# Kernel optimization log

Hardware: AMD Instinct MI355X
Metric: run time of the kernel (lower is better)

Reference implementation:

```python
import jax, jax.numpy as jnp
import numpy as np

EPS = 1e-5

def bn(x, g, b):
    # BatchNorm1d, training-mode batch statistics.
    axes = (0, 2) if x.ndim == 3 else (0,)
    m = jnp.mean(x, axis=axes, keepdims=True)
    v = jnp.var(x, axis=axes, keepdims=True)
    shape = (1, -1, 1) if x.ndim == 3 else (1, -1)
    return (x - m) / jnp.sqrt(v + EPS) * g.reshape(shape) + b.reshape(shape)

def conv1(x, w):
    # 1x1 conv1d == channel matmul: w [O,C], x [B,C,N]
    return jnp.einsum('oc,bcn->bon', w, x)

def knn_cov(x, local_idx, k):
    # x: [B,C,N], local_idx: [B,N] bool (local=True branch)
    B, C, N = x.shape
    xx = jnp.sum(x * x, axis=1, keepdims=True)          # [B,1,N]
    inner = -2.0 * jnp.einsum('bcn,bcm->bnm', x, x)      # [B,N,N]
    pd = -xx - inner - jnp.swapaxes(xx, 1, 2)            # neg sq dist [B,N,N]
    Min = jnp.min(pd, axis=-1)                           # [B,N]
    pd = jnp.where(local_idx[:, None, :], pd, Min[:, :, None])
    idx = jax.lax.top_k(jax.lax.stop_gradient(pd), k)[1]  # [B,N,k] nearest
    pts = jnp.swapaxes(x, 1, 2)                          # [B,N,C]
    knn_x = jax.vmap(lambda p, i: p[i])(pts, idx)        # [B,N,k,C]
    knn_x = knn_x - jnp.mean(knn_x, axis=2, keepdims=True)
    cov = jnp.einsum('bnkc,bnkd->bncd', knn_x, knn_x)    # [B,N,C,C]
    cov = cov.reshape(B, N, C * C).transpose(0, 2, 1)    # [B,C^2,N]
    return jnp.concatenate([x, cov], axis=1)             # [B,C+C^2,N]

def setup_inputs() -> dict:
    key = jax.random.key(0)
    ks = jax.random.split(key, 16)
    B, C, N, k = 4, 3, 8192, 20
    emb = 1024
    d = {}
    d['x'] = jax.random.normal(ks[0], (B, C, N), dtype=jnp.float32)
    d['local_idx'] = jax.random.randint(ks[1], (B, N), 0, 2) > 0
    d['k'] = k
    cin = C + C * C  # 12
    d['w1'] = jax.random.normal(ks[2], (64, cin), jnp.float32) * 0.1
    d['w2'] = jax.random.normal(ks[3], (64, 64), jnp.float32) * 0.1
    d['w3'] = jax.random.normal(ks[4], (64, 64), jnp.float32) * 0.1
    d['w4'] = jax.random.normal(ks[5], (128, 64), jnp.float32) * 0.1
    d['w5'] = jax.random.normal(ks[6], (emb, 128), jnp.float32) * 0.05
    for i, c in zip(range(1, 6), [64, 64, 64, 128, emb]):
        d[f'g{i}'] = jnp.ones((c,), jnp.float32)
        d[f'b{i}'] = jnp.zeros((c,), jnp.float32)
    d['lw1'] = jax.random.normal(ks[7], (512, emb), jnp.float32) * 0.03
    d['g6'] = jnp.ones((512,), jnp.float32)
    d['b6'] = jnp.zeros((512,), jnp.float32)
    d['lw2'] = jax.random.normal(ks[8], (4, 512), jnp.float32) * 0.05
    d['lb2'] = jnp.zeros((4,), jnp.float32)
    return d

def reference(x, local_idx, k, w1, w2, w3, w4, w5,
              g1, b1, g2, b2, g3, b3, g4, b4, g5, b5,
              lw1, g6, b6, lw2, lb2):
    h = knn_cov(x, local_idx, k)                 # [B,12,N]
    h = jax.nn.relu(bn(conv1(h, w1), g1, b1))
    h = jax.nn.relu(bn(conv1(h, w2), g2, b2))
    h = jax.nn.relu(bn(conv1(h, w3), g3, b3))
    h = jax.nn.relu(bn(conv1(h, w4), g4, b4))
    h = jax.nn.relu(bn(conv1(h, w5), g5, b5))    # [B,emb,N]
    h = jnp.max(h, axis=2)                        # global max pool [B,emb]
    h = jax.nn.relu(bn(h @ lw1.T, g6, b6))        # [B,512]
    # dropout: identity at eval
    return h @ lw2.T + lb2                        # [B,4]
```

## Files before the change

kernel.cpp:

```cpp
#include <hip/hip_runtime.h>

constexpr int BB = 4, NN = 8192, KNB = 20;
constexpr int BN_ = BB * NN;
constexpr float EPSV = 1e-5f;

constexpr size_t OFF_MODE  = 0;
constexpr size_t OFF_PCNT  = 16;
constexpr size_t OFF_PL    = 64;
constexpr size_t OFF_M0 = OFF_PL + 131072;
constexpr size_t OFF_S0 = OFF_M0 + 12;
constexpr size_t OFF_M1 = OFF_S0 + 144;
constexpr size_t OFF_S1 = OFF_M1 + 64;
constexpr size_t OFF_M2 = OFF_S1 + 64 * 64;
constexpr size_t OFF_S2 = OFF_M2 + 64;
constexpr size_t OFF_M3 = OFF_S2 + 64 * 64;
constexpr size_t OFF_S3 = OFF_M3 + 64;
constexpr size_t OFF_M4 = OFF_S3 + 64 * 64;
constexpr size_t OFF_S4 = OFF_M4 + 128;
constexpr size_t OFF_POOL = OFF_S4 + 128 * 128;
constexpr size_t OFF_ZEND = OFF_POOL + BB * 1024;
constexpr size_t OFF_A1 = OFF_ZEND;
constexpr size_t OFF_B1 = OFF_A1 + 64;
constexpr size_t OFF_A2 = OFF_B1 + 64;
constexpr size_t OFF_B2 = OFF_A2 + 64;
constexpr size_t OFF_A3 = OFF_B2 + 64;
constexpr size_t OFF_B3 = OFF_A3 + 64;
constexpr size_t OFF_A4 = OFF_B3 + 64;
constexpr size_t OFF_B4 = OFF_A4 + 128;
constexpr size_t OFF_A5 = OFF_B4 + 128;
constexpr size_t OFF_B5 = OFF_A5 + 1024;
constexpr size_t OFF_SH = OFF_B5 + 1024;
constexpr size_t OFF_WT1 = OFF_SH + BB * 512;
constexpr size_t OFF_WT2 = OFF_WT1 + 768;
constexpr size_t OFF_WT3 = OFF_WT2 + 4096;
constexpr size_t OFF_WT4 = OFF_WT3 + 4096;
constexpr size_t OFF_WT5_RAW = OFF_WT4 + 8192;
constexpr size_t OFF_WT5 = (OFF_WT5_RAW + 63) & ~size_t(63);
constexpr size_t OFF_H0_RAW = OFF_WT5 + 1024 * 128;
constexpr size_t OFF_H0 = (OFF_H0_RAW + 63) & ~size_t(63);
constexpr size_t OFF_H1 = OFF_H0 + (size_t)BB * 12 * NN;
constexpr size_t OFF_H2 = OFF_H1 + (size_t)BB * 64 * NN;
constexpr size_t OFF_H3 = OFF_H1;
constexpr size_t OFF_H4 = OFF_H2 + (size_t)BB * 64 * NN;
constexpr size_t OFF_P64  = OFF_H4;
constexpr size_t OFF_P128 = OFF_H1;
constexpr size_t WS_FLOATS = OFF_H4 + (size_t)BB * 128 * NN;

__device__ inline float dist3(const float4 c, float x0, float x1, float x2) {
  const float d0 = c.x - x0, d1 = c.y - x1, d2 = c.z - x2;
  return __builtin_fmaf(d0, d0, __builtin_fmaf(d1, d1, d2 * d2));
}

__global__ __launch_bounds__(256) void k_prep(const unsigned int* __restrict__ li32,
                                              int* __restrict__ mode,
                                              int* __restrict__ pcnt,
                                              float4* __restrict__ pl,
                                              const float* __restrict__ x) {
  const int b = blockIdx.x;
  const int t = threadIdx.x;
  const int lane = t & 63;
  const int w = t >> 6;
  __shared__ int s_wc[4];
  __shared__ int s_base;
  __shared__ int s_any;
  if (t == 0) { s_base = 0; s_any = 0; }
  __syncthreads();
  unsigned int any = 0;
  for (int i = t; i < 2048; i += 256) any |= (li32[b * 2048 + i] > 1u) ? 1u : 0u;
  if (any) atomicOr(&s_any, 1);
  __syncthreads();
  const int md = s_any;
  if (b == 0 && t == 0) *mode = md;
  const unsigned char* p8 = (const unsigned char*)li32;
  const float* __restrict__ xb = x + (size_t)b * 3 * NN;
  for (int j0 = 0; j0 < NN; j0 += 256) {
    const int m = j0 + t;
    const int f = md ? (p8[b * NN + m] != 0) : (li32[b * NN + m] != 0);
    const unsigned long long mask = __ballot(f);
    const int pos = __popcll(mask & ((1ull << lane) - 1ull));
    if (lane == 0) s_wc[w] = (int)__popcll(mask);
    __syncthreads();
    int off = s_base;
    for (int ww = 0; ww < w; ++ww) off += s_wc[ww];
    const int tot = s_wc[0] + s_wc[1] + s_wc[2] + s_wc[3];
    if (f) pl[(size_t)b * NN + off + pos] =
        make_float4(xb[m], xb[NN + m], xb[2 * NN + m], __int_as_float(m));
    __syncthreads();
    if (t == 0) s_base += tot;
    __syncthreads();
  }
  if (t == 0) pcnt[b] = s_base;
}

__global__ void k_wtall(const float* __restrict__ w1, const float* __restrict__ w2,
                        const float* __restrict__ w3, const float* __restrict__ w4,
                        const float* __restrict__ w5, float* __restrict__ wt1,
                        float* __restrict__ wt2, float* __restrict__ wt3,
                        float* __restrict__ wt4, float* __restrict__ wt5) {
  const int i = blockIdx.x * 256 + threadIdx.x;
  if (i < 768)        { const int o = i / 12,  c = i % 12;  wt1[c * 64 + o]  = w1[i]; }
  else if (i < 4864)  { const int j = i - 768;  const int o = j >> 6, c = j & 63;  wt2[c * 64 + o]  = w2[j]; }
  else if (i < 8960)  { const int j = i - 4864; const int o = j >> 6, c = j & 63;  wt3[c * 64 + o]  = w3[j]; }
  else if (i < 17152) { const int j = i - 8960; const int o = j >> 6, c = j & 63;  wt4[c * 128 + o] = w4[j]; }
  else if (i < 148224){ const int j = i - 17152;const int o = j >> 7, c = j & 127; wt5[c * 1024 + o] = w5[j]; }
}

__global__ __launch_bounds__(512) void k_knn(const float* __restrict__ x,
                                             const float4* __restrict__ pl,
                                             const int* __restrict__ pcnt,
                                             float* __restrict__ h0) {
  const int blk  = blockIdx.x;
  const int b    = blk >> 7;
  const int tile = blk & 127;
  const int t    = threadIdx.x;
  const int lane = t & 63;
  const int w    = __builtin_amdgcn_readfirstlane(t >> 6);
  const int n    = tile * 64 + lane;

  __shared__ float s_pool[8 * 64 * 21];
  __shared__ float s_T[64];
  __shared__ float s_red[64][13];
  __shared__ int   s_tc[64];
  __shared__ int   s_ti[64][16];
  float* __restrict__ s_dbuf = s_pool;

  const float* __restrict__ xb  = x + (size_t)b * 3 * NN;
  const float4* __restrict__ plb = pl + (size_t)b * NN;
  const int cnt = pcnt[b];
  const float xn0 = xb[n], xn1 = xb[NN + n], xn2 = xb[2 * NN + n];

  const int jlo = (cnt * w) >> 3;
  const int jhi = (cnt * (w + 1)) >> 3;

  float tk[KNB];
#pragma unroll
  for (int i = 0; i < KNB; ++i) tk[i] = 3.0e38f;

  {
    float thr = 3.0e38f;
    int bc = 0;
    for (int j = jlo; j < jhi; ++j) {
      const float4 c = plb[j];
      const float d = dist3(c, xn0, xn1, xn2);
      if (d < thr) { s_dbuf[bc * 512 + t] = d; ++bc; }
      if (__any(bc == 8)) {
        for (int i = 0; i < bc; ++i) {
          float dv = s_dbuf[i * 512 + t];
          if (dv < tk[KNB - 1]) {
#pragma unroll
            for (int q2 = 0; q2 < KNB; ++q2) {
              const float lo = fminf(tk[q2], dv);
              dv = fmaxf(tk[q2], dv);
              tk[q2] = lo;
            }
          }
        }
        bc = 0;
        thr = tk[KNB - 1];
      }
    }
    for (int i = 0; i < bc; ++i) {
      float dv = s_dbuf[i * 512 + t];
      if (dv < tk[KNB - 1]) {
#pragma unroll
        for (int q2 = 0; q2 < KNB; ++q2) {
          const float lo = fminf(tk[q2], dv);
          dv = fmaxf(tk[q2], dv);
          tk[q2] = lo;
        }
      }
    }
  }
  __syncthreads();

  {
    const int base = (w * 64 + lane) * 21;
#pragma unroll
    for (int i = 0; i < KNB; ++i) s_pool[base + i] = tk[i];
    s_pool[base + KNB] = 3.0e38f;
  }
  __syncthreads();

  if (w == 0) {
    int i0 = 0, i1 = 0, i2 = 0, i3 = 0, i4 = 0, i5 = 0, i6 = 0, i7 = 0;
    float T = 0.f;
    for (int c = 0; c < KNB; ++c) {
      const float v0 = s_pool[(0 * 64 + lane) * 21 + i0];
      const float v1 = s_pool[(1 * 64 + lane) * 21 + i1];
      const float v2 = s_pool[(2 * 64 + lane) * 21 + i2];
      const float v3 = s_pool[(3 * 64 + lane) * 21 + i3];
      const float v4 = s_pool[(4 * 64 + lane) * 21 + i4];
      const float v5 = s_pool[(5 * 64 + lane) * 21 + i5];
      const float v6 = s_pool[(6 * 64 + lane) * 21 + i6];
      const float v7 = s_pool[(7 * 64 + lane) * 21 + i7];
      float best = fminf(fminf(fminf(v0, v1), fminf(v2, v3)),
                         fminf(fminf(v4, v5), fminf(v6, v7)));
      int adv, taken;
      adv = (v0 == best) ? 1 : 0;           i0 += adv; taken = adv;
      adv = (!taken && v1 == best) ? 1 : 0; i1 += adv; taken |= adv;
      adv = (!taken && v2 == best) ? 1 : 0; i2 += adv; taken |= adv;
      adv = (!taken && v3 == best) ? 1 : 0; i3 += adv; taken |= adv;
      adv = (!taken && v4 == best) ? 1 : 0; i4 += adv; taken |= adv;
      adv = (!taken && v5 == best) ? 1 : 0; i5 += adv; taken |= adv;
      adv = (!taken && v6 == best) ? 1 : 0; i6 += adv; taken |= adv;
      adv = (!taken && v7 == best) ? 1 : 0; i7 += adv;
      T = best;
    }
    s_T[lane] = T;
    s_tc[lane] = 0;
  }
  __syncthreads();
  const float T = s_T[lane];

  float sx = 0, sy = 0, sz = 0;
  float xx = 0, xy = 0, xz = 0, yy = 0, yz = 0, zz = 0;
  float clf = 0;
#pragma unroll 2
  for (int j = jlo; j < jhi; ++j) {
    const float4 c = plb[j];
    const float d = dist3(c, xn0, xn1, xn2);
    if (d < T) {
      clf += 1.f;
      sx += c.x; sy += c.y; sz += c.z;
      xx = __builtin_fmaf(c.x, c.x, xx);
      xy = __builtin_fmaf(c.x, c.y, xy);
      xz = __builtin_fmaf(c.x, c.z, xz);
      yy = __builtin_fmaf(c.y, c.y, yy);
      yz = __builtin_fmaf(c.y, c.z, yz);
      zz = __builtin_fmaf(c.z, c.z, zz);
    } else if (d == T) {
      const int pos = atomicAdd(&s_tc[lane], 1);
      if (pos < 16) s_ti[lane][pos] = __float_as_int(c.w);
    }
  }
  __syncthreads();
  {
    const int base = (w * 64 + lane) * 13;
    s_pool[base + 0] = sx; s_pool[base + 1] = sy; s_pool[base + 2] = sz;
    s_pool[base + 3] = xx; s_pool[base + 4] = xy; s_pool[base + 5] = xz;
    s_pool[base + 6] = yy; s_pool[base + 7] = yz; s_pool[base + 8] = zz;
    s_pool[base + 9] = clf;
  }
  __syncthreads();
  {
    const int q = t & 63, a = t >> 6;
    float s = 0.f;
#pragma unroll
    for (int wv = 0; wv < 8; ++wv) s += s_pool[(wv * 64 + q) * 13 + a];
    s_red[q][a] = s;
    if (a < 2) {
      const int a2 = a + 8;
      float s2 = 0.f;
#pragma unroll
      for (int wv = 0; wv < 8; ++wv) s2 += s_pool[(wv * 64 + q) * 13 + a2];
      s_red[q][a2] = s2;
    }
  }
  __syncthreads();

  if (w == 0) {
    float fsx = s_red[lane][0], fsy = s_red[lane][1], fsz = s_red[lane][2];
    float fxx = s_red[lane][3], fxy = s_red[lane][4], fxz = s_red[lane][5];
    float fyy = s_red[lane][6], fyz = s_red[lane][7], fzz = s_red[lane][8];
    const int cl = (int)s_red[lane][9];
    const int r = KNB - cl;
    const int tc = min(s_tc[lane], 16);
    int kk = cl;
    int prev = -1;
    for (int s = 0; s < r; ++s) {
      int best = 0x7fffffff;
      for (int u = 0; u < tc; ++u) {
        const int mi = s_ti[lane][u];
        if (mi > prev && mi < best) best = mi;
      }
      if (best == 0x7fffffff) break;
      const float px = xb[best], py = xb[NN + best], pz = xb[2 * NN + best];
      fsx += px; fsy += py; fsz += pz;
      fxx = __builtin_fmaf(px, px, fxx);
      fxy = __builtin_fmaf(px, py, fxy);
      fxz = __builtin_fmaf(px, pz, fxz);
      fyy = __builtin_fmaf(py, py, fyy);
      fyz = __builtin_fmaf(py, pz, fyz);
      fzz = __builtin_fmaf(pz, pz, fzz);
      prev = best;
      ++kk;
    }
    const float kf = (float)max(kk, 1);
    const float inv = 1.0f / kf;
    const float mx = fsx * inv, my = fsy * inv, mz = fsz * inv;
    const float c00 = fxx - kf * mx * mx;
    const float c01 = fxy - kf * mx * my;
    const float c02 = fxz - kf * mx * mz;
    const float c11 = fyy - kf * my * my;
    const float c12 = fyz - kf * my * mz;
    const float c22 = fzz - kf * mz * mz;
    float* __restrict__ op = h0 + (size_t)b * 12 * NN + n;
    op[0] = xn0; op[(size_t)NN] = xn1; op[(size_t)2 * NN] = xn2;
    op[(size_t)3 * NN] = c00; op[(size_t)4 * NN]  = c01; op[(size_t)5 * NN]  = c02;
    op[(size_t)6 * NN] = c01; op[(size_t)7 * NN]  = c11; op[(size_t)8 * NN]  = c12;
    op[(size_t)9 * NN] = c02; op[(size_t)10 * NN] = c12; op[(size_t)11 * NN] = c22;
  }
}

template <int C>
__global__ __launch_bounds__(256) void k_stats_small(const float* __restrict__ h,
                                                     float* __restrict__ mo,
                                                     float* __restrict__ So) {
  constexpr int NP  = C * (C + 1) / 2;
  constexpr int KPT = (NP + 255) / 256;
  __shared__ float tile[C][65];
  const int t = threadIdx.x;
  float acc[KPT];
#pragma unroll
  for (int e = 0; e < KPT; ++e) acc[e] = 0.f;
  float accm = 0.f;
  for (int tl = blockIdx.x; tl < BN_ / 64; tl += gridDim.x) {
    const int b  = tl >> 7;
    const int p0 = (tl & 127) * 64;
    for (int idx = t; idx < C * 64; idx += 256) {
      const int c = idx >> 6, p = idx & 63;
      tile[c][p] = h[((size_t)b * C + c) * NN + p0 + p];
    }
    __syncthreads();
    {
      int ii = 0, rem = t;
#pragma unroll
      for (int e = 0; e < KPT; ++e) {
        const int lin = t + 256 * e;
        if (lin < NP) {
          while (rem >= C - ii) { rem -= C - ii; ++ii; }
          const int jj = ii + rem;
          float s = 0.f;
#pragma unroll 8
          for (int p = 0; p < 64; ++p) s = __builtin_fmaf(tile[ii][p], tile[jj][p], s);
          acc[e] += s;
        }
        rem += 256;
      }
    }
    if (t < C) {
      float s = 0.f;
#pragma unroll 8
      for (int p = 0; p < 64; ++p) s += tile[t][p];
      accm += s;
    }
    __syncthreads();
  }
  {
    int ii = 0, rem = t;
#pragma unroll
    for (int e = 0; e < KPT; ++e) {
      const int lin = t + 256 * e;
      if (lin < NP) {
        while (rem >= C - ii) { rem -= C - ii; ++ii; }
        atomicAdd(&So[ii * C + ii + rem], acc[e]);
      }
      rem += 256;
    }
  }
  if (t < C) atomicAdd(&mo[t], accm);
}

template <int C>
__global__ __launch_bounds__(512) void k_stats(const float* __restrict__ h,
                                               float* __restrict__ part) {
  constexpr int G      = (C == 128) ? 8 : 4;
  constexpr int NPB    = 136 * G * G;
  constexpr int ROWLEN = NPB + C;
  constexpr int STR    = C + 4;
  __shared__ float ht[128][STR];
  __shared__ float red[136][G * G];
  const int t   = threadIdx.x;
  const int blk = blockIdx.x;
  const int b   = blk >> 6;
  const int p0  = (blk & 63) * 128;
  for (int i = t; i < C * 128; i += 512) {
    const int c = i >> 7, p = i & 127;
    ht[p][c] = h[((size_t)b * C + c) * NN + p0 + p];
  }
  __syncthreads();
  const int s  = t >> 8;
  const int pb = t & 255;
  const int bi = pb & 15;
  const int bj = pb >> 4;
  const bool act = (bi <= bj);
  float acc[G * G];
#pragma unroll
  for (int g = 0; g < G * G; ++g) acc[g] = 0.f;
  if (act) {
    for (int p = s * 64; p < s * 64 + 64; ++p) {
      float a[G], bv[G];
      *(float4*)&a[0] = *(const float4*)&ht[p][bi * G];
      *(float4*)&bv[0] = *(const float4*)&ht[p][bj * G];
      if constexpr (G == 8) {
        *(float4*)&a[4] = *(const float4*)&ht[p][bi * G + 4];
        *(float4*)&bv[4] = *(const float4*)&ht[p][bj * G + 4];
      }
#pragma unroll
      for (int gi = 0; gi < G; ++gi)
#pragma unroll
        for (int gj = 0; gj < G; ++gj)
          acc[gi * G + gj] = __builtin_fmaf(a[gi], bv[gj], acc[gi * G + gj]);
    }
  }
  const int rank = bj * (bj + 1) / 2 + bi;
  if (s == 1 && act) {
#pragma unroll
    for (int g = 0; g < G * G; ++g) red[rank][g] = acc[g];
  }
  __syncthreads();
  float* __restrict__ prow = part + (size_t)blk * ROWLEN;
  if (s == 0 && act) {
#pragma unroll
    for (int g = 0; g < G * G; g += 4) {
      float4 v;
      v.x = acc[g + 0] + red[rank][g + 0];
      v.y = acc[g + 1] + red[rank][g + 1];
      v.z = acc[g + 2] + red[rank][g + 2];
      v.w = acc[g + 3] + red[rank][g + 3];
      *(float4*)&prow[rank * G * G + g] = v;
    }
  }
  if (t < C) {
    float sm = 0.f;
#pragma unroll 8
    for (int p = 0; p < 128; ++p) sm += ht[p][t];
    prow[NPB + t] = sm;
  }
}

template <int C>
__global__ __launch_bounds__(256) void k_sred(const float* __restrict__ part,
                                              float* __restrict__ mo,
                                              float* __restrict__ So) {
  constexpr int G      = (C == 128) ? 8 : 4;
  constexpr int GG     = G * G;
  constexpr int NPB    = 136 * GG;
  constexpr int ROWLEN = NPB + C;
  const int e = blockIdx.x * 256 + threadIdx.x;
  if (e >= ROWLEN) return;
  const float* __restrict__ p = part + e;
  float s = 0.f;
#pragma unroll 8
  for (int r = 0; r < 256; ++r) s += p[(size_t)r * ROWLEN];
  if (e < NPB) {
    const int rank = e / GG;
    const int g    = e - rank * GG;
    int bj = 0;
    while ((bj + 1) * (bj + 2) / 2 <= rank) ++bj;
    const int bi = rank - bj * (bj + 1) / 2;
    const int gi = g / G, gj = g - gi * G;
    So[(bi * G + gi) * C + (bj * G + gj)] = s;
  } else {
    mo[e - NPB] = s;
  }
}

template <int CIN, int COUT>
__global__ __launch_bounds__(256) void k_solve(const float* __restrict__ w, const float* __restrict__ g,
                        const float* __restrict__ bb, const float* __restrict__ m,
                        const float* __restrict__ S, float* __restrict__ A,
                        float* __restrict__ Bc) {
  const int wv   = threadIdx.x >> 6;
  const int lane = threadIdx.x & 63;
  const int o    = blockIdx.x * 4 + wv;
  if (o >= COUT) return;
  const float* __restrict__ wr = w + (size_t)o * CIN;
  float mu = 0.f;
  for (int i = lane; i < CIN; i += 64) mu = __builtin_fmaf(wr[i], m[i], mu);
  float e2 = 0.f;
#pragma unroll 4
  for (int lin = lane; lin < CIN * CIN; lin += 64) {
    const int i = lin / CIN;
    const int j = lin - i * CIN;
    const int lo = min(i, j), hi = max(i, j);
    e2 = __builtin_fmaf(wr[i] * wr[j], S[lo * CIN + hi], e2);
  }
#pragma unroll
  for (int off = 32; off >= 1; off >>= 1) {
    mu += __shfl_xor(mu, off, 64);
    e2 += __shfl_xor(e2, off, 64);
  }
  if (lane == 0) {
    mu *= (1.0f / BN_);
    e2 *= (1.0f / BN_);
    const float var = e2 - mu * mu;
    const float a = g[o] / sqrtf(var + EPSV);
    A[o] = a;
    Bc[o] = bb[o] - mu * a;
  }
}

template <int CIN, int COUT, bool POOL>
__global__ __launch_bounds__(256) void k_cgemm(const float* __restrict__ hin,
                                               const float* __restrict__ wt,
                                               const float* __restrict__ A,
                                               const float* __restrict__ Bc,
                                               float* __restrict__ outp) {
  constexpr int nOT = COUT / 64;
  __shared__ float tin[CIN][64];
  __shared__ float twt[CIN][64];
  const int blk = blockIdx.x;
  const int ot  = blk % nOT;
  const int pt  = blk / nOT;
  const int b   = pt >> 7;
  const int p0  = (pt & 127) * 64;
  const int o0  = ot * 64;
  const int t   = threadIdx.x;

  for (int i = t; i < CIN * 16; i += 256) {
    const int c = i >> 4, sgm = i & 15;
    *(float4*)&tin[c][sgm * 4] =
        *(const float4*)&hin[((size_t)b * CIN + c) * NN + p0 + sgm * 4];
    *(float4*)&twt[c][sgm * 4] =
        *(const float4*)&wt[(size_t)c * COUT + o0 + sgm * 4];
  }
  __syncthreads();

  const int to = t & 15;
  const int tp = t >> 4;
  float acc[4][4];
#pragma unroll
  for (int i = 0; i < 4; ++i)
#pragma unroll
    for (int j = 0; j < 4; ++j) acc[i][j] = 0.f;

#pragma unroll 4
  for (int c = 0; c < CIN; ++c) {
    const float4 av = *(const float4*)&twt[c][to * 4];
    const float4 pv = *(const float4*)&tin[c][tp * 4];
    const float aa[4] = {av.x, av.y, av.z, av.w};
    const float pp[4] = {pv.x, pv.y, pv.z, pv.w};
#pragma unroll
    for (int i = 0; i < 4; ++i)
#pragma unroll
      for (int j = 0; j < 4; ++j)
        acc[i][j] = __builtin_fmaf(aa[i], pp[j], acc[i][j]);
  }

  float Ao[4], Bo[4];
#pragma unroll
  for (int i = 0; i < 4; ++i) {
    Ao[i] = A[o0 + to * 4 + i];
    Bo[i] = Bc[o0 + to * 4 + i];
  }

  if constexpr (!POOL) {
#pragma unroll
    for (int i = 0; i < 4; ++i) {
      float4 vv;
      vv.x = fmaxf(__builtin_fmaf(acc[i][0], Ao[i], Bo[i]), 0.f);
      vv.y = fmaxf(__builtin_fmaf(acc[i][1], Ao[i], Bo[i]), 0.f);
      vv.z = fmaxf(__builtin_fmaf(acc[i][2], Ao[i], Bo[i]), 0.f);
      vv.w = fmaxf(__builtin_fmaf(acc[i][3], Ao[i], Bo[i]), 0.f);
      *(float4*)&outp[((size_t)b * COUT + o0 + to * 4 + i) * NN + p0 + tp * 4] = vv;
    }
  } else {
    float mx[4];
#pragma unroll
    for (int i = 0; i < 4; ++i) {
      float v0 = fmaxf(__builtin_fmaf(acc[i][0], Ao[i], Bo[i]), 0.f);
      float v1 = fmaxf(__builtin_fmaf(acc[i][1], Ao[i], Bo[i]), 0.f);
      float v2 = fmaxf(__builtin_fmaf(acc[i][2], Ao[i], Bo[i]), 0.f);
      float v3 = fmaxf(__builtin_fmaf(acc[i][3], Ao[i], Bo[i]), 0.f);
      float m = fmaxf(fmaxf(v0, v1), fmaxf(v2, v3));
      m = fmaxf(m, __shfl_xor(m, 16, 64));
      m = fmaxf(m, __shfl_xor(m, 32, 64));
      mx[i] = m;
    }
    float* s_part = &twt[0][0];
    __syncthreads();
    if ((t & 48) == 0) {
      const int w = t >> 6;
#pragma unroll
      for (int i = 0; i < 4; ++i) s_part[w * 64 + to * 4 + i] = mx[i];
    }
    __syncthreads();
    if (t < 64) {
      const float mm = fmaxf(fmaxf(s_part[t], s_part[64 + t]),
                             fmaxf(s_part[128 + t], s_part[192 + t]));
      atomicMax((int*)outp + (size_t)b * 1024 + o0 + t, __float_as_int(mm));
    }
  }
}

__global__ __launch_bounds__(256) void k_head1(const float* __restrict__ pooled, const float* __restrict__ lw1,
                        const float* __restrict__ g6, const float* __restrict__ b6,
                        float* __restrict__ sh) {
  const int wv   = threadIdx.x >> 6;
  const int lane = threadIdx.x & 63;
  const int o    = blockIdx.x * 4 + wv;
  const float* __restrict__ wr = lw1 + (size_t)o * 1024;
  float y0 = 0, y1 = 0, y2 = 0, y3 = 0;
  for (int c = lane; c < 1024; c += 64) {
    const float wvv = wr[c];
    y0 = __builtin_fmaf(wvv, pooled[c], y0);
    y1 = __builtin_fmaf(wvv, pooled[1024 + c], y1);
    y2 = __builtin_fmaf(wvv, pooled[2048 + c], y2);
    y3 = __builtin_fmaf(wvv, pooled[3072 + c], y3);
  }
#pragma unroll
  for (int off = 32; off >= 1; off >>= 1) {
    y0 += __shfl_xor(y0, off, 64);
    y1 += __shfl_xor(y1, off, 64);
    y2 += __shfl_xor(y2, off, 64);
    y3 += __shfl_xor(y3, off, 64);
  }
  if (lane == 0) {
    const float mu = 0.25f * (y0 + y1 + y2 + y3);
    const float d0 = y0 - mu, d1 = y1 - mu, d2 = y2 - mu, d3 = y3 - mu;
    const float var = 0.25f * (d0 * d0 + d1 * d1 + d2 * d2 + d3 * d3);
    const float a = g6[o] / sqrtf(var + EPSV);
    const float bc = b6[o];
    sh[o]        = fmaxf(__builtin_fmaf(d0, a, bc), 0.f);
    sh[512 + o]  = fmaxf(__builtin_fmaf(d1, a, bc), 0.f);
    sh[1024 + o] = fmaxf(__builtin_fmaf(d2, a, bc), 0.f);
    sh[1536 + o] = fmaxf(__builtin_fmaf(d3, a, bc), 0.f);
  }
}

__global__ void k_head2(const float* __restrict__ sh, const float* __restrict__ lw2,
                        const float* __restrict__ lb2, float* __restrict__ out) {
  const int wv   = threadIdx.x >> 6;
  const int lane = threadIdx.x & 63;
  float s0 = 0, s1 = 0, s2 = 0, s3 = 0;
  for (int c = lane; c < 512; c += 64) {
    const float h = sh[wv * 512 + c];
    s0 = __builtin_fmaf(lw2[c], h, s0);
    s1 = __builtin_fmaf(lw2[512 + c], h, s1);
    s2 = __builtin_fmaf(lw2[1024 + c], h, s2);
    s3 = __builtin_fmaf(lw2[1536 + c], h, s3);
  }
#pragma unroll
  for (int off = 32; off >= 1; off >>= 1) {
    s0 += __shfl_xor(s0, off, 64);
    s1 += __shfl_xor(s1, off, 64);
    s2 += __shfl_xor(s2, off, 64);
    s3 += __shfl_xor(s3, off, 64);
  }
  if (lane == 0) {
    out[wv * 4 + 0] = s0 + lb2[0];
    out[wv * 4 + 1] = s1 + lb2[1];
    out[wv * 4 + 2] = s2 + lb2[2];
    out[wv * 4 + 3] = s3 + lb2[3];
  }
}

extern "C" void kernel_launch(void* const* d_in, const int* in_sizes, int n_in,
                              void* d_out, int out_size, void* d_ws, size_t ws_size,
                              hipStream_t stream) {
  (void)in_sizes; (void)n_in; (void)out_size; (void)ws_size;
  const float* x    = (const float*)d_in[0];
  const void*  lidx = d_in[1];
  const float* w1 = (const float*)d_in[3];
  const float* w2 = (const float*)d_in[4];
  const float* w3 = (const float*)d_in[5];
  const float* w4 = (const float*)d_in[6];
  const float* w5 = (const float*)d_in[7];
  const float* g1 = (const float*)d_in[8],  *b1 = (const float*)d_in[9];
  const float* g2 = (const float*)d_in[10], *b2 = (const float*)d_in[11];
  const float* g3 = (const float*)d_in[12], *b3 = (const float*)d_in[13];
  const float* g4 = (const float*)d_in[14], *b4 = (const float*)d_in[15];
  const float* g5 = (const float*)d_in[16], *b5 = (const float*)d_in[17];
  const float* lw1 = (const float*)d_in[18];
  const float* g6 = (const float*)d_in[19], *b6 = (const float*)d_in[20];
  const float* lw2 = (const float*)d_in[21], *lb2 = (const float*)d_in[22];
  float* out = (float*)d_out;
  float* ws  = (float*)d_ws;

  hipMemsetAsync(ws + OFF_M0, 0, (OFF_ZEND - OFF_M0) * sizeof(float), stream);

  k_prep<<<4, 256, 0, stream>>>((const unsigned int*)lidx, (int*)(ws + OFF_MODE),
                                (int*)(ws + OFF_PCNT), (float4*)(ws + OFF_PL), x);
  k_wtall<<<579, 256, 0, stream>>>(w1, w2, w3, w4, w5, ws + OFF_WT1, ws + OFF_WT2,
                                   ws + OFF_WT3, ws + OFF_WT4, ws + OFF_WT5);
  k_knn<<<512, 512, 0, stream>>>(x, (const float4*)(ws + OFF_PL),
                                 (const int*)(ws + OFF_PCNT), ws + OFF_H0);

  k_stats_small<12><<<128, 256, 0, stream>>>(ws + OFF_H0, ws + OFF_M0, ws + OFF_S0);
  k_solve<12, 64><<<16, 256, 0, stream>>>(w1, g1, b1, ws + OFF_M0, ws + OFF_S0,
                                          ws + OFF_A1, ws + OFF_B1);
  k_cgemm<12, 64, false><<<512, 256, 0, stream>>>(ws + OFF_H0, ws + OFF_WT1,
                                                  ws + OFF_A1, ws + OFF_B1, ws + OFF_H1);

  k_stats<64><<<256, 512, 0, stream>>>(ws + OFF_H1, ws + OFF_P64);
  k_sred<64><<<9, 256, 0, stream>>>(ws + OFF_P64, ws + OFF_M1, ws + OFF_S1);
  k_solve<64, 64><<<16, 256, 0, stream>>>(w2, g2, b2, ws + OFF_M1, ws + OFF_S1,
                                          ws + OFF_A2, ws + OFF_B2);
  k_cgemm<64, 64, false><<<512, 256, 0, stream>>>(ws + OFF_H1, ws + OFF_WT2,
                                                  ws + OFF_A2, ws + OFF_B2, ws + OFF_H2);

  k_stats<64><<<256, 512, 0, stream>>>(ws + OFF_H2, ws + OFF_P64);
  k_sred<64><<<9, 256, 0, stream>>>(ws + OFF_P64, ws + OFF_M2, ws + OFF_S2);
  k_solve<64, 64><<<16, 256, 0, stream>>>(w3, g3, b3, ws + OFF_M2, ws + OFF_S2,
                                          ws + OFF_A3, ws + OFF_B3);
  k_cgemm<64, 64, false><<<512, 256, 0, stream>>>(ws + OFF_H2, ws + OFF_WT3,
                                                  ws + OFF_A3, ws + OFF_B3, ws + OFF_H3);

  k_stats<64><<<256, 512, 0, stream>>>(ws + OFF_H3, ws + OFF_P64);
  k_sred<64><<<9, 256, 0, stream>>>(ws + OFF_P64, ws + OFF_M3, ws + OFF_S3);
  k_solve<64, 128><<<32, 256, 0, stream>>>(w4, g4, b4, ws + OFF_M3, ws + OFF_S3,
                                           ws + OFF_A4, ws + OFF_B4);
  k_cgemm<64, 128, false><<<1024, 256, 0, stream>>>(ws + OFF_H3, ws + OFF_WT4,
                                                    ws + OFF_A4, ws + OFF_B4, ws + OFF_H4);

  k_stats<128><<<256, 512, 0, stream>>>(ws + OFF_H4, ws + OFF_P128);
  k_sred<128><<<35, 256, 0, stream>>>(ws + OFF_P128, ws + OFF_M4, ws + OFF_S4);
  k_solve<128, 1024><<<256, 256, 0, stream>>>(w5, g5, b5, ws + OFF_M4, ws + OFF_S4,
                                              ws + OFF_A5, ws + OFF_B5);
  k_cgemm<128, 1024, true><<<8192, 256, 0, stream>>>(ws + OFF_H4, ws + OFF_WT5,
                                                     ws + OFF_A5, ws + OFF_B5, ws + OFF_POOL);

  k_head1<<<128, 256, 0, stream>>>(ws + OFF_POOL, lw1, g6, b6, ws + OFF_SH);
  k_head2<<<1, 256, 0, stream>>>(ws + OFF_SH, lw2, lb2, out);
}
```

Measured before the change: 609.0 us.

## Compact kNN candidates before accumulation and add 128x64-tiled pooled final conv

The kNN second pass now only records the indices of candidates within the threshold into shared memory and processes them in batches of eight. This avoids running the divergent accumulate branch on every point and reads tie points from the packed float4 array. The last 128->1024 conv with max-pool becomes a dedicated kernel. Each thread computes an 8x4 register tile over 128 output channels, staging input in 64-channel chunks, which halves the number of blocks and the repeated reads of the input. The batching adds __any checks and shared-memory traffic, and the bigger tile raises register pressure.

```diff
diff --git a/kernel.cpp b/kernel.cpp
--- a/kernel.cpp
+++ b/kernel.cpp
@@ -122,7 +122,8 @@
   __shared__ float s_red[64][13];
   __shared__ int   s_tc[64];
   __shared__ int   s_ti[64][16];
-  float* __restrict__ s_dbuf = s_pool;
+  float* __restrict__ s_dbuf  = s_pool;
+  int*   __restrict__ s_dbufi = (int*)s_pool;
 
   const float* __restrict__ xb  = x + (size_t)b * 3 * NN;
   const float4* __restrict__ plb = pl + (size_t)b * NN;
@@ -215,22 +216,70 @@
   float sx = 0, sy = 0, sz = 0;
   float xx = 0, xy = 0, xz = 0, yy = 0, yz = 0, zz = 0;
   float clf = 0;
-#pragma unroll 2
-  for (int j = jlo; j < jhi; ++j) {
-    const float4 c = plb[j];
-    const float d = dist3(c, xn0, xn1, xn2);
-    if (d < T) {
-      clf += 1.f;
-      sx += c.x; sy += c.y; sz += c.z;
-      xx = __builtin_fmaf(c.x, c.x, xx);
-      xy = __builtin_fmaf(c.x, c.y, xy);
-      xz = __builtin_fmaf(c.x, c.z, xz);
-      yy = __builtin_fmaf(c.y, c.y, yy);
-      yz = __builtin_fmaf(c.y, c.z, yz);
-      zz = __builtin_fmaf(c.z, c.z, zz);
-    } else if (d == T) {
-      const int pos = atomicAdd(&s_tc[lane], 1);
-      if (pos < 16) s_ti[lane][pos] = __float_as_int(c.w);
+  {
+    s_dbufi[t] = jlo;
+    int bc = 0;
+    for (int j = jlo; j < jhi; ++j) {
+      const float4 c = plb[j];
+      const float d = dist3(c, xn0, xn1, xn2);
+      if (d <= T) { s_dbufi[bc * 512 + t] = j; ++bc; }
+      if (__any(bc == 8)) {
+        int jj[8]; float4 cc[8];
+#pragma unroll
+        for (int i = 0; i < 8; ++i) {
+          const int slot = (i < bc) ? i : 0;
+          jj[i] = s_dbufi[slot * 512 + t];
+          cc[i] = plb[jj[i]];
+        }
+#pragma unroll
+        for (int i = 0; i < 8; ++i) {
+          if (i < bc) {
+            const float d2 = dist3(cc[i], xn0, xn1, xn2);
+            if (d2 < T) {
+              clf += 1.f;
+              sx += cc[i].x; sy += cc[i].y; sz += cc[i].z;
+              xx = __builtin_fmaf(cc[i].x, cc[i].x, xx);
+              xy = __builtin_fmaf(cc[i].x, cc[i].y, xy);
+              xz = __builtin_fmaf(cc[i].x, cc[i].z, xz);
+              yy = __builtin_fmaf(cc[i].y, cc[i].y, yy);
+              yz = __builtin_fmaf(cc[i].y, cc[i].z, yz);
+              zz = __builtin_fmaf(cc[i].z, cc[i].z, zz);
+            } else {
+              const int pos = atomicAdd(&s_tc[lane], 1);
+              if (pos < 16) s_ti[lane][pos] = jj[i];
+            }
+          }
+        }
+        bc = 0;
+      }
+    }
+    if (bc > 0) {
+      int jj[8]; float4 cc[8];
+#pragma unroll
+      for (int i = 0; i < 8; ++i) {
+        const int slot = (i < bc) ? i : 0;
+        jj[i] = s_dbufi[slot * 512 + t];
+        cc[i] = plb[jj[i]];
+      }
+#pragma unroll
+      for (int i = 0; i < 8; ++i) {
+        if (i < bc) {
+          const float d2 = dist3(cc[i], xn0, xn1, xn2);
+          if (d2 < T) {
+            clf += 1.f;
+            sx += cc[i].x; sy += cc[i].y; sz += cc[i].z;
+            xx = __builtin_fmaf(cc[i].x, cc[i].x, xx);
+            xy = __builtin_fmaf(cc[i].x, cc[i].y, xy);
+            xz = __builtin_fmaf(cc[i].x, cc[i].z, xz);
+            yy = __builtin_fmaf(cc[i].y, cc[i].y, yy);
+            yz = __builtin_fmaf(cc[i].y, cc[i].z, yz);
+            zz = __builtin_fmaf(cc[i].z, cc[i].z, zz);
+          } else {
+            const int pos = atomicAdd(&s_tc[lane], 1);
+            if (pos < 16) s_ti[lane][pos] = jj[i];
+          }
+        }
+      }
     }
   }
   __syncthreads();
@@ -270,18 +319,18 @@
     for (int s = 0; s < r; ++s) {
       int best = 0x7fffffff;
       for (int u = 0; u < tc; ++u) {
-        const int mi = s_ti[lane][u];
-        if (mi > prev && mi < best) best = mi;
+        const int mi2 = s_ti[lane][u];
+        if (mi2 > prev && mi2 < best) best = mi2;
       }
       if (best == 0x7fffffff) break;
-      const float px = xb[best], py = xb[NN + best], pz = xb[2 * NN + best];
-      fsx += px; fsy += py; fsz += pz;
-      fxx = __builtin_fmaf(px, px, fxx);
-      fxy = __builtin_fmaf(px, py, fxy);
-      fxz = __builtin_fmaf(px, pz, fxz);
-      fyy = __builtin_fmaf(py, py, fyy);
-      fyz = __builtin_fmaf(py, pz, fyz);
-      fzz = __builtin_fmaf(pz, pz, fzz);
+      const float4 pp = plb[best];
+      fsx += pp.x; fsy += pp.y; fsz += pp.z;
+      fxx = __builtin_fmaf(pp.x, pp.x, fxx);
+      fxy = __builtin_fmaf(pp.x, pp.y, fxy);
+      fxz = __builtin_fmaf(pp.x, pp.z, fxz);
+      fyy = __builtin_fmaf(pp.y, pp.y, fyy);
+      fyz = __builtin_fmaf(pp.y, pp.z, fyz);
+      fzz = __builtin_fmaf(pp.z, pp.z, fzz);
       prev = best;
       ++kk;
     }
@@ -491,7 +540,7 @@
   }
 }
 
-template <int CIN, int COUT, bool POOL>
+template <int CIN, int COUT>
 __global__ __launch_bounds__(256) void k_cgemm(const float* __restrict__ hin,
                                                const float* __restrict__ wt,
                                                const float* __restrict__ A,
@@ -538,49 +587,95 @@
         acc[i][j] = __builtin_fmaf(aa[i], pp[j], acc[i][j]);
   }
 
-  float Ao[4], Bo[4];
 #pragma unroll
   for (int i = 0; i < 4; ++i) {
-    Ao[i] = A[o0 + to * 4 + i];
-    Bo[i] = Bc[o0 + to * 4 + i];
-  }
-
-  if constexpr (!POOL) {
-#pragma unroll
-    for (int i = 0; i < 4; ++i) {
-      float4 vv;
-      vv.x = fmaxf(__builtin_fmaf(acc[i][0], Ao[i], Bo[i]), 0.f);
-      vv.y = fmaxf(__builtin_fmaf(acc[i][1], Ao[i], Bo[i]), 0.f);
-      vv.z = fmaxf(__builtin_fmaf(acc[i][2], Ao[i], Bo[i]), 0.f);
-      vv.w = fmaxf(__builtin_fmaf(acc[i][3], Ao[i], Bo[i]), 0.f);
-      *(float4*)&outp[((size_t)b * COUT + o0 + to * 4 + i) * NN + p0 + tp * 4] = vv;
-    }
-  } else {
-    float mx[4];
-#pragma unroll
-    for (int i = 0; i < 4; ++i) {
-      float v0 = fmaxf(__builtin_fmaf(acc[i][0], Ao[i], Bo[i]), 0.f);
-      float v1 = fmaxf(__builtin_fmaf(acc[i][1], Ao[i], Bo[i]), 0.f);
-      float v2 = fmaxf(__builtin_fmaf(acc[i][2], Ao[i], Bo[i]), 0.f);
-      float v3 = fmaxf(__builtin_fmaf(acc[i][3], Ao[i], Bo[i]), 0.f);
-      float m = fmaxf(fmaxf(v0, v1), fmaxf(v2, v3));
-      m = fmaxf(m, __shfl_xor(m, 16, 64));
-      m = fmaxf(m, __shfl_xor(m, 32, 64));
-      mx[i] = m;
-    }
-    float* s_part = &twt[0][0];
+    const int o = o0 + to * 4 + i;
+    const float Ao = A[o], Bo = Bc[o];
+    float4 vv;
+    vv.x = fmaxf(__builtin_fmaf(acc[i][0], Ao, Bo), 0.f);
+    vv.y = fmaxf(__builtin_fmaf(acc[i][1], Ao, Bo), 0.f);
+    vv.z = fmaxf(__builtin_fmaf(acc[i][2], Ao, Bo), 0.f);
+    vv.w = fmaxf(__builtin_fmaf(acc[i][3], Ao, Bo), 0.f);
+    *(float4*)&outp[((size_t)b * COUT + o) * NN + p0 + tp * 4] = vv;
+  }
+}
+
+__global__ __launch_bounds__(256) void k_cgemm5(const float* __restrict__ h4,
+                                                const float* __restrict__ wt,
+                                                const float* __restrict__ A,
+                                                const float* __restrict__ Bc,
+                                                float* __restrict__ pooled) {
+  __shared__ float tin[64][64];
+  __shared__ float twt[64][128];
+  const int blk = blockIdx.x;
+  const int ot  = blk & 7;
+  const int pt  = blk >> 3;
+  const int b   = pt >> 7;
+  const int p0  = (pt & 127) * 64;
+  const int o0  = ot * 128;
+  const int t   = threadIdx.x;
+  const int to  = t & 15;
+  const int tp  = t >> 4;
+
+  float acc[8][4];
+#pragma unroll
+  for (int i = 0; i < 8; ++i)
+#pragma unroll
+    for (int j = 0; j < 4; ++j) acc[i][j] = 0.f;
+
+  for (int kc = 0; kc < 128; kc += 64) {
+    if (kc) __syncthreads();
+    for (int i = t; i < 64 * 16; i += 256) {
+      const int c = i >> 4, sg = i & 15;
+      *(float4*)&tin[c][sg * 4] =
+          *(const float4*)&h4[((size_t)b * 128 + kc + c) * NN + p0 + sg * 4];
+    }
+    for (int i = t; i < 64 * 32; i += 256) {
+      const int c = i >> 5, sg = i & 31;
+      *(float4*)&twt[c][sg * 4] =
+          *(const float4*)&wt[(size_t)(kc + c) * 1024 + o0 + sg * 4];
+    }
     __syncthreads();
-    if ((t & 48) == 0) {
-      const int w = t >> 6;
-#pragma unroll
-      for (int i = 0; i < 4; ++i) s_part[w * 64 + to * 4 + i] = mx[i];
-    }
-    __syncthreads();
-    if (t < 64) {
-      const float mm = fmaxf(fmaxf(s_part[t], s_part[64 + t]),
-                             fmaxf(s_part[128 + t], s_part[192 + t]));
-      atomicMax((int*)outp + (size_t)b * 1024 + o0 + t, __float_as_int(mm));
-    }
+#pragma unroll 2
+    for (int c = 0; c < 64; ++c) {
+      float w8[8], p4[4];
+      *(float4*)&w8[0] = *(const float4*)&twt[c][to * 8];
+      *(float4*)&w8[4] = *(const float4*)&twt[c][to * 8 + 4];
+      *(float4*)&p4[0] = *(const float4*)&tin[c][tp * 4];
+#pragma unroll
+      for (int i = 0; i < 8; ++i)
+#pragma unroll
+        for (int j = 0; j < 4; ++j)
+          acc[i][j] = __builtin_fmaf(w8[i], p4[j], acc[i][j]);
+    }
+  }
+
+  float mx[8];
+#pragma unroll
+  for (int i = 0; i < 8; ++i) {
+    const int o = o0 + to * 8 + i;
+    const float a = A[o], bo = Bc[o];
+    float v0 = fmaxf(__builtin_fmaf(acc[i][0], a, bo), 0.f);
+    float v1 = fmaxf(__builtin_fmaf(acc[i][1], a, bo), 0.f);
+    float v2 = fmaxf(__builtin_fmaf(acc[i][2], a, bo), 0.f);
+    float v3 = fmaxf(__builtin_fmaf(acc[i][3], a, bo), 0.f);
+    float m = fmaxf(fmaxf(v0, v1), fmaxf(v2, v3));
+    m = fmaxf(m, __shfl_xor(m, 16, 64));
+    m = fmaxf(m, __shfl_xor(m, 32, 64));
+    mx[i] = m;
+  }
+  float* s_part = &twt[0][0];
+  __syncthreads();
+  const int lane = t & 63, w = t >> 6;
+  if (lane < 16) {
+#pragma unroll
+    for (int i = 0; i < 8; ++i) s_part[w * 128 + to * 8 + i] = mx[i];
+  }
+  __syncthreads();
+  if (t < 128) {
+    const float mm = fmaxf(fmaxf(s_part[t], s_part[128 + t]),
+                           fmaxf(s_part[256 + t], s_part[384 + t]));
+    atomicMax((int*)pooled + (size_t)b * 1024 + o0 + t, __float_as_int(mm));
   }
 }
 
@@ -680,36 +775,36 @@
   k_stats_small<12><<<128, 256, 0, stream>>>(ws + OFF_H0, ws + OFF_M0, ws + OFF_S0);
   k_solve<12, 64><<<16, 256, 0, stream>>>(w1, g1, b1, ws + OFF_M0, ws + OFF_S0,
                                           ws + OFF_A1, ws + OFF_B1);
-  k_cgemm<12, 64, false><<<512, 256, 0, stream>>>(ws + OFF_H0, ws + OFF_WT1,
-                                                  ws + OFF_A1, ws + OFF_B1, ws + OFF_H1);
+  k_cgemm<12, 64><<<512, 256, 0, stream>>>(ws + OFF_H0, ws + OFF_WT1,
+                                           ws + OFF_A1, ws + OFF_B1, ws + OFF_H1);
 
   k_stats<64><<<256, 512, 0, stream>>>(ws + OFF_H1, ws + OFF_P64);
   k_sred<64><<<9, 256, 0, stream>>>(ws + OFF_P64, ws + OFF_M1, ws + OFF_S1);
   k_solve<64, 64><<<16, 256, 0, stream>>>(w2, g2, b2, ws + OFF_M1, ws + OFF_S1,
                                           ws + OFF_A2, ws + OFF_B2);
-  k_cgemm<64, 64, false><<<512, 256, 0, stream>>>(ws + OFF_H1, ws + OFF_WT2,
-                                                  ws + OFF_A2, ws + OFF_B2, ws + OFF_H2);
+  k_cgemm<64, 64><<<512, 256, 0, stream>>>(ws + OFF_H1, ws + OFF_WT2,
+                                           ws + OFF_A2, ws + OFF_B2, ws + OFF_H2);
 
   k_stats<64><<<256, 512, 0, stream>>>(ws + OFF_H2, ws + OFF_P64);
   k_sred<64><<<9, 256, 0, stream>>>(ws + OFF_P64, ws + OFF_M2, ws + OFF_S2);
   k_solve<64, 64><<<16, 256, 0, stream>>>(w3, g3, b3, ws + OFF_M2, ws + OFF_S2,
                                           ws + OFF_A3, ws + OFF_B3);
-  k_cgemm<64, 64, false><<<512, 256, 0, stream>>>(ws + OFF_H2, ws + OFF_WT3,
-                                                  ws + OFF_A3, ws + OFF_B3, ws + OFF_H3);
+  k_cgemm<64, 64><<<512, 256, 0, stream>>>(ws + OFF_H2, ws + OFF_WT3,
+                                           ws + OFF_A3, ws + OFF_B3, ws + OFF_H3);
 
   k_stats<64><<<256, 512, 0, stream>>>(ws + OFF_H3, ws + OFF_P64);
   k_sred<64><<<9, 256, 0, stream>>>(ws + OFF_P64, ws + OFF_M3, ws + OFF_S3);
   k_solve<64, 128><<<32, 256, 0, stream>>>(w4, g4, b4, ws + OFF_M3, ws + OFF_S3,
                                            ws + OFF_A4, ws + OFF_B4);
-  k_cgemm<64, 128, false><<<1024, 256, 0, stream>>>(ws + OFF_H3, ws + OFF_WT4,
-                                                    ws + OFF_A4, ws + OFF_B4, ws + OFF_H4);
+  k_cgemm<64, 128><<<1024, 256, 0, stream>>>(ws + OFF_H3, ws + OFF_WT4,
+                                             ws + OFF_A4, ws + OFF_B4, ws + OFF_H4);
 
   k_stats<128><<<256, 512, 0, stream>>>(ws + OFF_H4, ws + OFF_P128);
   k_sred<128><<<35, 256, 0, stream>>>(ws + OFF_P128, ws + OFF_M4, ws + OFF_S4);
   k_solve<128, 1024><<<256, 256, 0, stream>>>(w5, g5, b5, ws + OFF_M4, ws + OFF_S4,
                                               ws + OFF_A5, ws + OFF_B5);
-  k_cgemm<128, 1024, true><<<8192, 256, 0, stream>>>(ws + OFF_H4, ws + OFF_WT5,
-                                                     ws + OFF_A5, ws + OFF_B5, ws + OFF_POOL);
+  k_cgemm5<<<4096, 256, 0, stream>>>(ws + OFF_H4, ws + OFF_WT5,
+                                     ws + OFF_A5, ws + OFF_B5, ws + OFF_POOL);
 
   k_head1<<<128, 256, 0, stream>>>(ws + OFF_POOL, lw1, g6, b6, ws + OFF_SH);
   k_head2<<<1, 256, 0, stream>>>(ws + OFF_SH, lw2, lb2, out);
```

Measured after the change: 586.6 us. 3.7% less time.
